# Kernel optimization log

Measured on AMD Instinct MI355X. Metric: run time of the kernel, lower is better.

The kernel has to match this reference:

```python
import jax, jax.numpy as jnp
import numpy as np

EMBED = 1024
HEADS = 16
HEAD_DIM = EMBED // HEADS


def setup_inputs() -> dict:
    key = jax.random.key(0)
    ks = jax.random.split(key, 11)
    B, S = 4, 2048
    scale = 1.0 / np.sqrt(EMBED)
    inp = {
        "query": jax.random.normal(ks[0], (B, S, EMBED), dtype=jnp.float32),
        "key": jax.random.normal(ks[1], (B, S, EMBED), dtype=jnp.float32),
        "value": jax.random.normal(ks[2], (B, S, EMBED), dtype=jnp.float32),
        "Wq": jax.random.normal(ks[3], (EMBED, EMBED), dtype=jnp.float32) * scale,
        "bq": jnp.zeros((EMBED,), dtype=jnp.float32),
        "Wk": jax.random.normal(ks[4], (EMBED, EMBED), dtype=jnp.float32) * scale,
        "bk": jnp.zeros((EMBED,), dtype=jnp.float32),
        "Wv": jax.random.normal(ks[5], (EMBED, EMBED), dtype=jnp.float32) * scale,
        "bv": jnp.zeros((EMBED,), dtype=jnp.float32),
        "Wo": jax.random.normal(ks[6], (EMBED, EMBED), dtype=jnp.float32) * scale,
        "bo": jnp.zeros((EMBED,), dtype=jnp.float32),
    }
    return inp


def _split_heads(x):
    # [B,S,E] -> [B,H,S,D]
    B, S, _ = x.shape
    return x.reshape(B, S, HEADS, HEAD_DIM).transpose(0, 2, 1, 3)


def reference(query, key, value, Wq, bq, Wk, bk, Wv, bv, Wo, bo):
    B, S, _ = query.shape
    q = _split_heads(query @ Wq.T + bq)   # [B,H,S,D]
    k = _split_heads(key @ Wk.T + bk)
    v = _split_heads(value @ Wv.T + bv)
    scores = jnp.einsum("bhqd,bhkd->bhqk", q, k) / jnp.sqrt(jnp.float32(HEAD_DIM))
    attn = jax.nn.softmax(scores, axis=-1)
    out = jnp.einsum("bhqk,bhkd->bhqd", attn, v)  # [B,H,S,D]
    out = out.transpose(0, 2, 1, 3).reshape(B, S, EMBED)
    return out @ Wo.T + bo
```

## Files before the change

### kernel.cpp

```cpp
#include <hip/hip_runtime.h>

typedef _Float16 f16;
typedef __attribute__((ext_vector_type(2))) __fp16 fp16x2_raw;
typedef __attribute__((ext_vector_type(4))) _Float16 f16x4;
typedef __attribute__((ext_vector_type(8))) _Float16 f16x8;
typedef __attribute__((ext_vector_type(4))) float f32x4;
typedef __attribute__((ext_vector_type(16))) float f32x16;
typedef __attribute__((ext_vector_type(2))) unsigned int u32x2;
typedef __attribute__((ext_vector_type(4))) unsigned int u32x4;

#define NB 4
#define NS 2048
#define NE 1024
#define NH 16
#define ND 64
#define NM (NB*NS)

__device__ __forceinline__ void gld16(const void* g, void* l) {
  __builtin_amdgcn_global_load_lds((const __attribute__((address_space(1))) unsigned int*)g,
                                   (__attribute__((address_space(3))) unsigned int*)l, 16, 0, 0);
}

__device__ __forceinline__ unsigned cvt2h(float a, float b) {
  fp16x2_raw r = __builtin_amdgcn_cvt_pkrtz(a, b);
  return __builtin_bit_cast(unsigned, r);
}

__device__ __forceinline__ void plswap(unsigned& a, unsigned& b) {
  asm volatile("v_permlane32_swap_b32 %0, %1" : "+v"(a), "+v"(b));
}

__global__ __launch_bounds__(256) void cvt_w(const float* __restrict__ s3, const float* __restrict__ s4,
                                             const float* __restrict__ s5, const float* __restrict__ s6,
                                             f16* __restrict__ dst) {
  const int W = NE*NE/4;
  const int total = 4*W;
  int idx = blockIdx.x * blockDim.x + threadIdx.x;
  int stride = gridDim.x * blockDim.x;
  for (int i = idx; i < total; i += stride) {
    const float* src; int off;
    if      (i <   W)   { src = s3; off = i; }
    else if (i < 2*W)   { src = s4; off = i - W; }
    else if (i < 3*W)   { src = s5; off = i - 2*W; }
    else                { src = s6; off = i - 3*W; }
    float4 v = ((const float4*)src)[off];
    f16x4 o;
    o[0] = (_Float16)v.x; o[1] = (_Float16)v.y; o[2] = (_Float16)v.z; o[3] = (_Float16)v.w;
    ((f16x4*)dst)[i] = o;
  }
}

template<bool AF32, bool OUTF32>
__global__ __launch_bounds__(256)
void gemm_bt(const void* __restrict__ Asrc, const f16* __restrict__ Bw,
             const float* __restrict__ bias, float* __restrict__ Cf,
             f16* __restrict__ Ch, int M, int N, int K)
{
  __shared__ __align__(16) f16 As[2*128*32];
  __shared__ __align__(16) f16 Bs[2*128*32];
  const int t = threadIdx.x;
  const int l = t & 63, w = t >> 6;
  const int wr = w >> 1, wc = w & 1;

  const int id = blockIdx.x + blockIdx.y * gridDim.x;
  const int xcd = id & 7, slot = id >> 3;
  const int m0 = (((slot >> 3) << 3) | xcd) * 128;
  const int n0 = (slot & 7) * 128;

  f32x4 acc[4][4];
  #pragma unroll
  for (int i = 0; i < 4; ++i)
    #pragma unroll
    for (int j = 0; j < 4; ++j)
      acc[i][j] = f32x4{0.f, 0.f, 0.f, 0.f};

  const int off0 = (w*2+0)*1024 + l*16;
  const int off1 = (w*2+1)*1024 + l*16;
  const int row0 = off0 >> 6, k0 = (off0 & 63) >> 1;
  const int row1 = off1 >> 6, k1 = (off1 & 63) >> 1;
  const f16*   a0h = (const f16*)Asrc   + (size_t)(m0+row0)*K + k0;
  const f16*   a1h = (const f16*)Asrc   + (size_t)(m0+row1)*K + k1;
  const float* a0f = (const float*)Asrc + (size_t)(m0+row0)*K + k0;
  const float* a1f = (const float*)Asrc + (size_t)(m0+row1)*K + k1;
  const f16* b0 = Bw + (size_t)(n0+row0)*K + k0;
  const f16* b1 = Bw + (size_t)(n0+row1)*K + k1;

  const int aoff = (wr*64 + (l&15))*32 + ((l>>4)<<3);
  const int boff = (wc*64 + (l&15))*32 + ((l>>4)<<3);

  gld16(b0, Bs + off0/2);
  gld16(b1, Bs + off1/2);
  if constexpr (AF32) {
    float4 x0 = *(const float4*)(a0f);
    float4 x1 = *(const float4*)(a0f + 4);
    float4 y0 = *(const float4*)(a1f);
    float4 y1 = *(const float4*)(a1f + 4);
    u32x4 wa, wb;
    wa[0] = cvt2h(x0.x, x0.y); wa[1] = cvt2h(x0.z, x0.w);
    wa[2] = cvt2h(x1.x, x1.y); wa[3] = cvt2h(x1.z, x1.w);
    wb[0] = cvt2h(y0.x, y0.y); wb[1] = cvt2h(y0.z, y0.w);
    wb[2] = cvt2h(y1.x, y1.y); wb[3] = cvt2h(y1.z, y1.w);
    *(u32x4*)(As + off0/2) = wa;
    *(u32x4*)(As + off1/2) = wb;
  } else {
    gld16(a0h, As + off0/2);
    gld16(a1h, As + off1/2);
  }
  asm volatile("s_waitcnt vmcnt(0)" ::: "memory");
  __syncthreads();

  const int NK = K / 32;
  for (int ksi = 0; ksi < NK; ++ksi) {
    const int cur = ksi & 1, nxt = cur ^ 1;
    float4 x0, x1, y0, y1;
    if (ksi < NK-1) {
      const int kt = (ksi+1) * 32;
      gld16(b0 + kt, Bs + nxt*4096 + off0/2);
      gld16(b1 + kt, Bs + nxt*4096 + off1/2);
      if constexpr (AF32) {
        x0 = *(const float4*)(a0f + kt);
        x1 = *(const float4*)(a0f + kt + 4);
        y0 = *(const float4*)(a1f + kt);
        y1 = *(const float4*)(a1f + kt + 4);
      } else {
        gld16(a0h + kt, As + nxt*4096 + off0/2);
        gld16(a1h + kt, As + nxt*4096 + off1/2);
      }
    }
    const f16* Ac = As + cur*4096;
    const f16* Bc = Bs + cur*4096;
    f16x8 af[4], bf[4];
    #pragma unroll
    for (int i = 0; i < 4; ++i) af[i] = *(const f16x8*)(Ac + aoff + i*512);
    #pragma unroll
    for (int j = 0; j < 4; ++j) bf[j] = *(const f16x8*)(Bc + boff + j*512);
    #pragma unroll
    for (int i = 0; i < 4; ++i)
      #pragma unroll
      for (int j = 0; j < 4; ++j)
        acc[i][j] = __builtin_amdgcn_mfma_f32_16x16x32_f16(af[i], bf[j], acc[i][j], 0, 0, 0);
    asm volatile("s_waitcnt vmcnt(0)" ::: "memory");
    if constexpr (AF32) {
      if (ksi < NK-1) {
        u32x4 wa, wb;
        wa[0] = cvt2h(x0.x, x0.y); wa[1] = cvt2h(x0.z, x0.w);
        wa[2] = cvt2h(x1.x, x1.y); wa[3] = cvt2h(x1.z, x1.w);
        wb[0] = cvt2h(y0.x, y0.y); wb[1] = cvt2h(y0.z, y0.w);
        wb[2] = cvt2h(y1.x, y1.y); wb[3] = cvt2h(y1.z, y1.w);
        *(u32x4*)(As + nxt*4096 + off0/2) = wa;
        *(u32x4*)(As + nxt*4096 + off1/2) = wb;
      }
    }
    __syncthreads();
  }

  #pragma unroll
  for (int j = 0; j < 4; ++j) {
    const int col = n0 + wc*64 + j*16 + (l & 15);
    const float bb = bias[col];
    #pragma unroll
    for (int i = 0; i < 4; ++i) {
      const int rowb = m0 + wr*64 + i*16 + ((l>>4)<<2);
      #pragma unroll
      for (int r = 0; r < 4; ++r) {
        float v = acc[i][j][r] + bb;
        if constexpr (OUTF32) Cf[(size_t)(rowb+r)*N + col] = v;
        else                  Ch[(size_t)(rowb+r)*N + col] = (f16)v;
      }
    }
  }
}

__global__ __launch_bounds__(256, 4)
void attn_kernel(const f16* __restrict__ Q, const f16* __restrict__ K,
                 const f16* __restrict__ V, f16* __restrict__ O)
{
  __shared__ __align__(16) f16 S_lds[16384];

  const int t = threadIdx.x, l = t & 63, w = t >> 6;
  const int lq = l & 31, hi = l >> 5;

  const int lin = blockIdx.x + (blockIdx.y << 4);
  const int xcd = lin & 7, jj = lin >> 3;
  const int bh = xcd * 8 + (jj >> 4);
  const int qt = jj & 15;
  const int b = bh >> 4, h = bh & 15;
  const size_t base = (size_t)b * NS * NE + (size_t)h * ND;
  const int q = qt*128 + w*32 + lq;

  f16x8 bq[4];
  #pragma unroll
  for (int ks = 0; ks < 4; ++ks)
    bq[ks] = *(const f16x8*)&Q[base + (size_t)q*NE + ks*16 + hi*8];
  asm volatile("s_waitcnt vmcnt(0)" ::: "memory");

  f32x16 o[2];
  #pragma unroll
  for (int dt = 0; dt < 2; ++dt)
    #pragma unroll
    for (int r = 0; r < 16; ++r) o[dt][r] = 0.f;
  float m2 = -3e38f, lsum = 0.f;
  const float K2 = 0.125f * 1.44269504089f;

  const int krow0 = w*16 + (l>>3);
  const int kgran = ((l&7) ^ (l>>3)) * 8;
  const f16* kSrc0 = K + base + (size_t)krow0*NE + kgran;
  const f16* kSrc1 = kSrc0 + (size_t)8*NE;
  const f16* vSrc = V + base + (size_t)l*NE + w*16;

  const size_t tileAdv = (size_t)64 * NE;
  const int kd0 = (w*2+0)*512 + l*8;
  const int kd1 = (w*2+1)*512 + l*8;

  f16x8 va, vb;
  {
    gld16(kSrc0, &S_lds[0] + kd0);
    gld16(kSrc1, &S_lds[0] + kd1);
    va = *(const f16x8*)(vSrc);
    vb = *(const f16x8*)(vSrc + 8);
    asm volatile("s_waitcnt vmcnt(0)" ::: "memory");
    char* vt0 = (char*)&S_lds[4096];
    #pragma unroll
    for (int i = 0; i < 8; ++i) {
      const int d0 = w*16 + i, d1 = w*16 + 8 + i;
      *(f16*)(vt0 + ((d0*128 + l*2) ^ ((i & 7) << 4))) = va[i];
      *(f16*)(vt0 + ((d1*128 + l*2) ^ ((i & 7) << 4))) = vb[i];
    }
  }
  __syncthreads();

  for (int it = 0; it < 32; ++it) {
    const int cur = it & 1, nb = cur ^ 1;
    const char* ksb = (const char*)(&S_lds[cur*8192]);
    const char* vtb = (const char*)(&S_lds[cur*8192 + 4096]);

    if (it < 31) {
      const size_t g = (size_t)(it+1) * tileAdv;
      gld16(kSrc0 + g, &S_lds[nb*8192] + kd0);
      gld16(kSrc1 + g, &S_lds[nb*8192] + kd1);
      va = *(const f16x8*)(vSrc + g);
      vb = *(const f16x8*)(vSrc + g + 8);
    }

    f32x16 s[2];
    #pragma unroll
    for (int ct = 0; ct < 2; ++ct)
      #pragma unroll
      for (int r = 0; r < 16; ++r) s[ct][r] = 0.f;
    __builtin_amdgcn_s_setprio(1);
    #pragma unroll
    for (int ct = 0; ct < 2; ++ct) {
      const int krow = ct*32 + lq;
      const int rswz = (krow & 7) << 4;
      #pragma unroll
      for (int ks = 0; ks < 4; ++ks) {
        f16x8 ak = *(const f16x8*)(ksb + ((krow*128 + ks*32 + hi*16) ^ rswz));
        s[ct] = __builtin_amdgcn_mfma_f32_32x32x16_f16(ak, bq[ks], s[ct], 0, 0, 0);
      }
    }
    __builtin_amdgcn_s_setprio(0);

    float mm[16];
    #pragma unroll
    for (int r = 0; r < 16; ++r) mm[r] = fmaxf(s[0][r], s[1][r]);
    #pragma unroll
    for (int st = 8; st > 0; st >>= 1)
      #pragma unroll
      for (int r = 0; r < st; ++r) mm[r] = fmaxf(mm[r], mm[r+st]);
    float mx = mm[0] * K2;
    mx = fmaxf(mx, __shfl_xor(mx, 32));

    if (__any(mx > m2 + 8.0f)) {
      const float mnew = fmaxf(m2, mx);
      const float alpha = __builtin_amdgcn_exp2f(m2 - mnew);
      m2 = mnew;
      lsum *= alpha;
      #pragma unroll
      for (int dt = 0; dt < 2; ++dt)
        #pragma unroll
        for (int r = 0; r < 16; ++r) o[dt][r] *= alpha;
    }

    float ps4[4] = {0.f, 0.f, 0.f, 0.f};
    #pragma unroll
    for (int ct = 0; ct < 2; ++ct)
      #pragma unroll
      for (int r = 0; r < 16; ++r) {
        float p = __builtin_amdgcn_exp2f(s[ct][r]*K2 - m2);
        s[ct][r] = p;
        ps4[r & 3] += p;
      }
    lsum += (ps4[0] + ps4[1]) + (ps4[2] + ps4[3]);

    f16x8 pa[4];
    #pragma unroll
    for (int ct = 0; ct < 2; ++ct) {
      unsigned wd[8];
      #pragma unroll
      for (int m = 0; m < 4; ++m)
        #pragma unroll
        for (int hh = 0; hh < 2; ++hh)
          wd[m*2 + hh] = cvt2h(s[ct][4*m + 2*hh], s[ct][4*m + 2*hh + 1]);
      #pragma unroll
      for (int ks2 = 0; ks2 < 2; ++ks2) {
        unsigned a0 = wd[(2*ks2)*2 + 0], b0 = wd[(2*ks2+1)*2 + 0];
        unsigned a1 = wd[(2*ks2)*2 + 1], b1 = wd[(2*ks2+1)*2 + 1];
        plswap(a0, b0);
        plswap(a1, b1);
        union { unsigned u[4]; f16x8 v; } pp;
        pp.u[0] = a0; pp.u[1] = a1; pp.u[2] = b0; pp.u[3] = b1;
        pa[ct*2 + ks2] = pp.v;
      }
    }

    __builtin_amdgcn_s_setprio(1);
    #pragma unroll
    for (int ks = 0; ks < 4; ++ks)
      #pragma unroll
      for (int dt = 0; dt < 2; ++dt) {
        const int drow = dt*32 + lq;
        f16x8 av = *(const f16x8*)(vtb + ((drow*128 + ks*32 + hi*16) ^ ((drow & 7) << 4)));
        o[dt] = __builtin_amdgcn_mfma_f32_32x32x16_f16(av, pa[ks], o[dt], 0, 0, 0);
      }
    __builtin_amdgcn_s_setprio(0);

    if (it < 31) {
      asm volatile("s_waitcnt vmcnt(0)" ::: "memory");
      char* vtn = (char*)(&S_lds[nb*8192 + 4096]);
      #pragma unroll
      for (int i = 0; i < 8; ++i) {
        const int d0 = w*16 + i, d1 = w*16 + 8 + i;
        *(f16*)(vtn + ((d0*128 + l*2) ^ ((i & 7) << 4))) = va[i];
        *(f16*)(vtn + ((d1*128 + l*2) ^ ((i & 7) << 4))) = vb[i];
      }
      __syncthreads();
    }
  }

  const float lt = lsum + __shfl_xor(lsum, 32);
  const float linv = 1.0f / lt;
  #pragma unroll
  for (int dt = 0; dt < 2; ++dt)
    #pragma unroll
    for (int m = 0; m < 4; ++m) {
      u32x2 st;
      st.x = cvt2h(o[dt][4*m+0]*linv, o[dt][4*m+1]*linv);
      st.y = cvt2h(o[dt][4*m+2]*linv, o[dt][4*m+3]*linv);
      const int d = dt*32 + 8*m + 4*hi;
      *(u32x2*)&O[base + (size_t)q*NE + d] = st;
    }
}

extern "C" void kernel_launch(void* const* d_in, const int* in_sizes, int n_in,
                              void* d_out, int out_size, void* d_ws, size_t ws_size,
                              hipStream_t stream)
{
  const float* q_in = (const float*)d_in[0];
  const float* k_in = (const float*)d_in[1];
  const float* v_in = (const float*)d_in[2];
  const float* Wq = (const float*)d_in[3];
  const float* bq = (const float*)d_in[4];
  const float* Wk = (const float*)d_in[5];
  const float* bk = (const float*)d_in[6];
  const float* Wv = (const float*)d_in[7];
  const float* bv = (const float*)d_in[8];
  const float* Wo = (const float*)d_in[9];
  const float* bo = (const float*)d_in[10];

  char* ws = (char*)d_ws;
  f16* Wq16 = (f16*)(ws + 50331648);
  f16* Wk16 = (f16*)(ws + 52428800);
  f16* Wv16 = (f16*)(ws + 54525952);
  f16* Wo16 = (f16*)(ws + 56623104);
  f16* Qp   = (f16*)(ws + 58720256);
  f16* Kp   = (f16*)(ws + 75497472);
  f16* Vp   = (f16*)(ws + 92274688);
  f16* Op   = (f16*)(ws + 109051904);

  cvt_w<<<1024, 256, 0, stream>>>(Wq, Wk, Wv, Wo, Wq16);

  dim3 gg(8, 64);
  gemm_bt<true,  false><<<gg, 256, 0, stream>>>(q_in, Wq16, bq, nullptr, Qp, NM, NE, NE);
  gemm_bt<true,  false><<<gg, 256, 0, stream>>>(k_in, Wk16, bk, nullptr, Kp, NM, NE, NE);
  gemm_bt<true,  false><<<gg, 256, 0, stream>>>(v_in, Wv16, bv, nullptr, Vp, NM, NE, NE);

  attn_kernel<<<dim3(16, 64), 256, 0, stream>>>(Qp, Kp, Vp, Op);

  gemm_bt<false, true><<<gg, 256, 0, stream>>>(Op, Wo16, bo, (float*)d_out, nullptr, NM, NE, NE);
}
```

Baseline: 238.9 us.

## Split attention along the KV dimension into two halves and add a combine kernel

The attention kernel now launches twice as many blocks, each covering half of the key/value sequence. Each block writes a partial normalized output plus its running max and sum, and a new combine kernel merges the two halves with a log-sum-exp reweighting. LDS double buffering is dropped in favour of a single buffer with synchronous loads, which halves shared memory to allow more resident blocks. This trades load/compute overlap and extra global traffic for the partials against more parallelism, and adds one kernel launch.

Result: slower. 269.1 us (+12.6%).

```diff
diff --git a/kernel.cpp b/kernel.cpp
--- a/kernel.cpp
+++ b/kernel.cpp
@@ -15,6 +15,7 @@
 #define NH 16
 #define ND 64
 #define NM (NB*NS)
+#define NROW (NB*NS*NH)
 
 __device__ __forceinline__ void gld16(const void* g, void* l) {
   __builtin_amdgcn_global_load_lds((const __attribute__((address_space(1))) unsigned int*)g,
@@ -173,9 +174,9 @@
 
 __global__ __launch_bounds__(256, 4)
 void attn_kernel(const f16* __restrict__ Q, const f16* __restrict__ K,
-                 const f16* __restrict__ V, f16* __restrict__ O)
+                 const f16* __restrict__ V, f16* __restrict__ Opart, float2* __restrict__ ml)
 {
-  __shared__ __align__(16) f16 S_lds[16384];
+  __shared__ __align__(16) f16 S_lds[8192];
 
   const int t = threadIdx.x, l = t & 63, w = t >> 6;
   const int lq = l & 31, hi = l >> 5;
@@ -184,14 +185,16 @@
   const int xcd = lin & 7, jj = lin >> 3;
   const int bh = xcd * 8 + (jj >> 4);
   const int qt = jj & 15;
+  const int bz = blockIdx.z;
   const int b = bh >> 4, h = bh & 15;
   const size_t base = (size_t)b * NS * NE + (size_t)h * ND;
-  const int q = qt*128 + w*32 + lq;
+  const int qrow = qt*128 + w*32 + lq;
+  const int koff = bz * (NS/2);
 
   f16x8 bq[4];
   #pragma unroll
   for (int ks = 0; ks < 4; ++ks)
-    bq[ks] = *(const f16x8*)&Q[base + (size_t)q*NE + ks*16 + hi*8];
+    bq[ks] = *(const f16x8*)&Q[base + (size_t)qrow*NE + ks*16 + hi*8];
   asm volatile("s_waitcnt vmcnt(0)" ::: "memory");
 
   f32x16 o[2];
@@ -204,43 +207,34 @@
 
   const int krow0 = w*16 + (l>>3);
   const int kgran = ((l&7) ^ (l>>3)) * 8;
-  const f16* kSrc0 = K + base + (size_t)krow0*NE + kgran;
+  const f16* kSrc0 = K + base + (size_t)(koff + krow0)*NE + kgran;
   const f16* kSrc1 = kSrc0 + (size_t)8*NE;
-  const f16* vSrc = V + base + (size_t)l*NE + w*16;
+  const f16* vSrc = V + base + (size_t)(koff + l)*NE + w*16;
+
+  f16* kDst0 = &S_lds[0] + (w*2+0)*512 + l*8;
+  f16* kDst1 = &S_lds[0] + (w*2+1)*512 + l*8;
+  const char* ksb = (const char*)&S_lds[0];
+  char* vtb = (char*)&S_lds[4096];
 
   const size_t tileAdv = (size_t)64 * NE;
-  const int kd0 = (w*2+0)*512 + l*8;
-  const int kd1 = (w*2+1)*512 + l*8;
-
-  f16x8 va, vb;
-  {
-    gld16(kSrc0, &S_lds[0] + kd0);
-    gld16(kSrc1, &S_lds[0] + kd1);
-    va = *(const f16x8*)(vSrc);
-    vb = *(const f16x8*)(vSrc + 8);
+
+  for (int it = 0; it < 16; ++it) {
+    const size_t g = (size_t)it * tileAdv;
+    __syncthreads();
+    gld16(kSrc0 + g, kDst0);
+    gld16(kSrc1 + g, kDst1);
+    {
+      f16x8 va = *(const f16x8*)(vSrc + g);
+      f16x8 vb = *(const f16x8*)(vSrc + g + 8);
+      #pragma unroll
+      for (int i = 0; i < 8; ++i) {
+        const int d0 = w*16 + i, d1 = w*16 + 8 + i;
+        *(f16*)(vtb + ((d0*128 + l*2) ^ ((i & 7) << 4))) = va[i];
+        *(f16*)(vtb + ((d1*128 + l*2) ^ ((i & 7) << 4))) = vb[i];
+      }
+    }
     asm volatile("s_waitcnt vmcnt(0)" ::: "memory");
-    char* vt0 = (char*)&S_lds[4096];
-    #pragma unroll
-    for (int i = 0; i < 8; ++i) {
-      const int d0 = w*16 + i, d1 = w*16 + 8 + i;
-      *(f16*)(vt0 + ((d0*128 + l*2) ^ ((i & 7) << 4))) = va[i];
-      *(f16*)(vt0 + ((d1*128 + l*2) ^ ((i & 7) << 4))) = vb[i];
-    }
-  }
-  __syncthreads();
-
-  for (int it = 0; it < 32; ++it) {
-    const int cur = it & 1, nb = cur ^ 1;
-    const char* ksb = (const char*)(&S_lds[cur*8192]);
-    const char* vtb = (const char*)(&S_lds[cur*8192 + 4096]);
-
-    if (it < 31) {
-      const size_t g = (size_t)(it+1) * tileAdv;
-      gld16(kSrc0 + g, &S_lds[nb*8192] + kd0);
-      gld16(kSrc1 + g, &S_lds[nb*8192] + kd1);
-      va = *(const f16x8*)(vSrc + g);
-      vb = *(const f16x8*)(vSrc + g + 8);
-    }
+    __syncthreads();
 
     f32x16 s[2];
     #pragma unroll
@@ -323,22 +317,11 @@
         o[dt] = __builtin_amdgcn_mfma_f32_32x32x16_f16(av, pa[ks], o[dt], 0, 0, 0);
       }
     __builtin_amdgcn_s_setprio(0);
-
-    if (it < 31) {
-      asm volatile("s_waitcnt vmcnt(0)" ::: "memory");
-      char* vtn = (char*)(&S_lds[nb*8192 + 4096]);
-      #pragma unroll
-      for (int i = 0; i < 8; ++i) {
-        const int d0 = w*16 + i, d1 = w*16 + 8 + i;
-        *(f16*)(vtn + ((d0*128 + l*2) ^ ((i & 7) << 4))) = va[i];
-        *(f16*)(vtn + ((d1*128 + l*2) ^ ((i & 7) << 4))) = vb[i];
-      }
-      __syncthreads();
-    }
   }
 
   const float lt = lsum + __shfl_xor(lsum, 32);
   const float linv = 1.0f / lt;
+  f16* Od = Opart + (size_t)bz * ((size_t)NM * NE);
   #pragma unroll
   for (int dt = 0; dt < 2; ++dt)
     #pragma unroll
@@ -347,8 +330,42 @@
       st.x = cvt2h(o[dt][4*m+0]*linv, o[dt][4*m+1]*linv);
       st.y = cvt2h(o[dt][4*m+2]*linv, o[dt][4*m+3]*linv);
       const int d = dt*32 + 8*m + 4*hi;
-      *(u32x2*)&O[base + (size_t)q*NE + d] = st;
-    }
+      *(u32x2*)&Od[base + (size_t)qrow*NE + d] = st;
+    }
+  if (hi == 0) {
+    const int rid = bh*NS + qrow;
+    ml[(size_t)bz*131072 + rid] = float2{m2, lt};
+  }
+}
+
+__global__ __launch_bounds__(256)
+void attn_combine(const f16* __restrict__ Opart, const float2* __restrict__ ml,
+                  f16* __restrict__ O)
+{
+  const int gid = blockIdx.x * 256 + threadIdx.x;
+  const int rid = gid >> 3;
+  const int dg  = (gid & 7) << 3;
+  const int bh = rid >> 11;
+  const int qrow = rid & (NS - 1);
+  const int b = bh >> 4, h = bh & 15;
+  const size_t addr = ((size_t)(b*NS + qrow))*NE + h*ND + dg;
+
+  const float2 a = ml[rid];
+  const float2 c = ml[131072 + rid];
+  const float ms = fmaxf(a.x, c.x);
+  const float w0 = __builtin_amdgcn_exp2f(a.x - ms) * a.y;
+  const float w1 = __builtin_amdgcn_exp2f(c.x - ms) * c.y;
+  const float inv = 1.0f / (w0 + w1);
+  const float c0 = w0 * inv, c1 = w1 * inv;
+
+  f16x8 o0 = *(const f16x8*)&Opart[addr];
+  f16x8 o1 = *(const f16x8*)&Opart[(size_t)NM*NE + addr];
+  u32x4 st;
+  #pragma unroll
+  for (int i = 0; i < 4; ++i)
+    st[i] = cvt2h((float)o0[2*i]*c0 + (float)o1[2*i]*c1,
+                  (float)o0[2*i+1]*c0 + (float)o1[2*i+1]*c1);
+  *(u32x4*)&O[addr] = st;
 }
 
 extern "C" void kernel_launch(void* const* d_in, const int* in_sizes, int n_in,
@@ -368,6 +385,8 @@
   const float* bo = (const float*)d_in[10];
 
   char* ws = (char*)d_ws;
+  f16*    Opart = (f16*)(ws + 0);
+  float2* mlb   = (float2*)(ws + 33554432);
   f16* Wq16 = (f16*)(ws + 50331648);
   f16* Wk16 = (f16*)(ws + 52428800);
   f16* Wv16 = (f16*)(ws + 54525952);
@@ -384,7 +403,8 @@
   gemm_bt<true,  false><<<gg, 256, 0, stream>>>(k_in, Wk16, bk, nullptr, Kp, NM, NE, NE);
   gemm_bt<true,  false><<<gg, 256, 0, stream>>>(v_in, Wv16, bv, nullptr, Vp, NM, NE, NE);
 
-  attn_kernel<<<dim3(16, 64), 256, 0, stream>>>(Qp, Kp, Vp, Op);
+  attn_kernel<<<dim3(16, 64, 2), 256, 0, stream>>>(Qp, Kp, Vp, Opart, mlb);
+  attn_combine<<<4096, 256, 0, stream>>>(Opart, mlb, Op);
 
   gemm_bt<false, true><<<gg, 256, 0, stream>>>(Op, Wo16, bo, (float*)d_out, nullptr, NM, NE, NE);
 }
```
